# Kernel tuning notes

Measured on AMD Instinct MI355X. Metric: run time of the kernel, lower is better.

## Reference

```python
import jax, jax.numpy as jnp
import numpy as np

DELTA = 1e-3  # inverse-distance kernel smoothing from NEC paper
NUM_NEIGHBOURS = 50


def setup_inputs() -> dict:
    key = jax.random.key(0)
    k1, k2, k3 = jax.random.split(key, 3)
    B, C, D = 1024, 500000, 64
    return {
        "keys": jax.random.normal(k1, (B, D), dtype=jnp.float32),
        "table_keys": jax.random.normal(k2, (C, D), dtype=jnp.float32),
        "table_values": jax.random.normal(k3, (C,), dtype=jnp.float32),
    }


def reference(keys, table_keys, table_values):
    # Brute-force kNN search: squared L2 distances [B, C]
    d2 = (
        jnp.sum(keys * keys, axis=1, keepdims=True)
        - 2.0 * (keys @ table_keys.T)
        + jnp.sum(table_keys * table_keys, axis=1)[None, :]
    )
    _, idx = jax.lax.top_k(-d2, NUM_NEIGHBOURS)  # [B, K] smallest distances

    neighbours = table_keys[idx]  # [B, K, D] gather
    # recompute exact squared distances against gathered neighbours
    sq = jnp.sum((keys[:, None, :] - neighbours) ** 2, axis=2)  # [B, K]
    w = 1.0 / (sq + DELTA)
    w = w / jnp.sum(w, axis=1, keepdims=True)
    v = table_values[idx]  # [B, K]
    return jnp.sum(w * v, axis=1)  # [B]
```

## Files before the change

kernel.cpp:

```cpp
#include <hip/hip_runtime.h>
#include <math.h>


#define DELTA_SMOOTH 1e-3f
#define K_NEIGH 50
#define MAXCAP 8192
#define SAMPLE 2048
#define SAMPLE_TARGET 6
#define NBINS 256
#define MARGIN 0.75f
#define MARGIN_Q 26
#define RPB 1024
#define QTILE 512
#define SDEPTH 8
#define LW 768
#define NQ 1024

typedef __attribute__((ext_vector_type(8))) short short8;
typedef __attribute__((ext_vector_type(4))) float f32x4;

__device__ __forceinline__ unsigned f2bf(float f) {
  unsigned u = __float_as_uint(f);
  return ((u + 0x7fffu + ((u >> 16) & 1u)) >> 16) & 0xffffu;
}

__global__ __launch_bounds__(256) void qthresh_kernel(
    const float* __restrict__ keys, const float* __restrict__ tk,
    float* __restrict__ thr, float* __restrict__ qnorm, int C) {
  int q = blockIdx.x;
  __shared__ __align__(16) float kq[64];
  __shared__ unsigned hist[NBINS];
  __shared__ float qn_sh;
  __shared__ unsigned wsum[4];
  __shared__ int bstar_sh;
  int tid = threadIdx.x;
  int lane = tid & 63;
  int wid = tid >> 6;
  if (tid < 64) kq[tid] = keys[(size_t)q * 64 + tid];
  hist[tid] = 0u;
  if (tid == 0) bstar_sh = NBINS - 1;
  __syncthreads();
  if (tid < 64) {
    float v = kq[tid];
    float s = v * v;
    #pragma unroll
    for (int off = 32; off > 0; off >>= 1) s += __shfl_down(s, off);
    if (tid == 0) qn_sh = s;
  }
  __syncthreads();
  float qn = qn_sh;
  int kc = lane & 3;
  const float4* kq4 = (const float4*)kq;
  float4 kf[4];
  #pragma unroll
  for (int j = 0; j < 4; ++j) kf[j] = kq4[kc * 4 + j];
  int S = SAMPLE < C ? SAMPLE : C;
  for (int r = wid * (S >> 2) + (lane >> 2); r < (wid + 1) * (S >> 2); r += 16) {
    const float4* trow = (const float4*)(tk + (size_t)r * 64 + kc * 16);
    float a0 = 0.f, a1 = 0.f, sq = 0.f;
    #pragma unroll
    for (int j = 0; j < 4; ++j) {
      float4 tvv = trow[j];
      float4 kv = kf[j];
      a0 += kv.x * tvv.x + kv.y * tvv.y;
      a1 += kv.z * tvv.z + kv.w * tvv.w;
      sq += tvv.x * tvv.x + tvv.y * tvv.y + tvv.z * tvv.z + tvv.w * tvv.w;
    }
    float s = a0 + a1;
    s += __shfl_xor(s, 1); s += __shfl_xor(s, 2);
    sq += __shfl_xor(sq, 1); sq += __shfl_xor(sq, 2);
    if (kc == 0) {
      float d2 = qn + sq - 2.f * s;
      int b = (int)d2;
      b = b < 0 ? 0 : (b > NBINS - 1 ? NBINS - 1 : b);
      atomicAdd(&hist[b], 1u);
    }
  }
  __syncthreads();
  unsigned h = hist[tid];
  unsigned p = h;
  #pragma unroll
  for (int off = 1; off < 64; off <<= 1) {
    unsigned v = __shfl_up(p, off);
    if (lane >= off) p += v;
  }
  if (lane == 63) wsum[wid] = p;
  __syncthreads();
  unsigned add = 0;
  for (int w2 = 0; w2 < wid; ++w2) add += wsum[w2];
  p += add;
  if (p >= (unsigned)SAMPLE_TARGET && p - h < (unsigned)SAMPLE_TARGET) bstar_sh = tid;
  __syncthreads();
  if (tid == 0) {
    thr[q] = (float)(bstar_sh + 1) + MARGIN - qn;
    qnorm[q] = qn;
  }
}

__global__ __launch_bounds__(512, 4) void filter_mfma_kernel(
    const float* __restrict__ keys, const float* __restrict__ tk,
    const float* __restrict__ thr, const float* __restrict__ qnorm,
    int* __restrict__ cnt, unsigned* __restrict__ candi, int C, int cap) {
  __shared__ float tnstage[64];
  __shared__ float thr_lds[QTILE];
  __shared__ float qn_lds[QTILE];
  __shared__ unsigned scnt[QTILE];
  __shared__ unsigned sbuf[QTILE * SDEPTH];
  __shared__ __align__(16) unsigned char bstage[64 * 128];

  int tid = threadIdx.x;
  int qt = blockIdx.x & 1;
  int chunk = blockIdx.x >> 1;
  int qbase = qt * QTILE;
  int rstart = chunk * RPB;

  thr_lds[tid] = thr[qbase + tid];
  qn_lds[tid] = qnorm[qbase + tid];
  scnt[tid] = 0u;

  int lane = tid & 63;
  int wq = tid >> 6;
  int l15 = lane & 15;
  int quad = lane >> 4;

  short8 afrag[4][2];
  #pragma unroll
  for (int mt = 0; mt < 4; ++mt) {
    const float* kp = keys + (size_t)(qbase + wq * 64 + mt * 16 + l15) * 64 + quad * 8;
    #pragma unroll
    for (int s = 0; s < 2; ++s) {
      float4 x = *(const float4*)(kp + s * 32);
      float4 y = *(const float4*)(kp + s * 32 + 4);
      short8 a;
      a[0] = (short)f2bf(x.x); a[1] = (short)f2bf(x.y);
      a[2] = (short)f2bf(x.z); a[3] = (short)f2bf(x.w);
      a[4] = (short)f2bf(y.x); a[5] = (short)f2bf(y.y);
      a[6] = (short)f2bf(y.z); a[7] = (short)f2bf(y.w);
      afrag[mt][s] = a;
    }
  }
  __syncthreads();

  float hq[4];
  #pragma unroll
  for (int mt = 0; mt < 4; ++mt) {
    float h0 = thr_lds[wq * 64 + mt * 16 + quad * 4 + 0];
    float h1 = thr_lds[wq * 64 + mt * 16 + quad * 4 + 1];
    float h2 = thr_lds[wq * 64 + mt * 16 + quad * 4 + 2];
    float h3 = thr_lds[wq * 64 + mt * 16 + quad * 4 + 3];
    hq[mt] = fmaxf(fmaxf(h0, h1), fmaxf(h2, h3));
  }

  int srow = tid >> 3;
  int scol = tid & 7;
  unsigned sbyte = (unsigned)(srow * 128 + ((scol ^ (srow & 7)) << 4));

  const int ITERS = RPB / 64;
  int r0 = rstart + srow; if (r0 > C - 1) r0 = C - 1;
  float4 pa = *(const float4*)(tk + (size_t)r0 * 64 + scol * 8);
  float4 pb = *(const float4*)(tk + (size_t)r0 * 64 + scol * 8 + 4);

  f32x4 zero4 = {0.f, 0.f, 0.f, 0.f};

  for (int it = 0; it < ITERS; ++it) {
    float part = pa.x * pa.x + pa.y * pa.y + pa.z * pa.z + pa.w * pa.w
               + pb.x * pb.x + pb.y * pb.y + pb.z * pb.z + pb.w * pb.w;
    part += __shfl_xor(part, 1);
    part += __shfl_xor(part, 2);
    part += __shfl_xor(part, 4);
    if ((tid & 7) == 0) tnstage[srow] = part;
    uint4 u;
    u.x = f2bf(pa.x) | (f2bf(pa.y) << 16);
    u.y = f2bf(pa.z) | (f2bf(pa.w) << 16);
    u.z = f2bf(pb.x) | (f2bf(pb.y) << 16);
    u.w = f2bf(pb.z) | (f2bf(pb.w) << 16);
    *(uint4*)(bstage + sbyte) = u;
    __syncthreads();
    if (it + 1 < ITERS) {
      int rn = rstart + (it + 1) * 64 + srow; if (rn > C - 1) rn = C - 1;
      pa = *(const float4*)(tk + (size_t)rn * 64 + scol * 8);
      pb = *(const float4*)(tk + (size_t)rn * 64 + scol * 8 + 4);
    }
    #pragma unroll
    for (int half = 0; half < 2; ++half) {
      short8 b[2][2];
      #pragma unroll
      for (int tt = 0; tt < 2; ++tt) {
        int nloc = half * 32 + tt * 16 + l15;
        #pragma unroll
        for (int s = 0; s < 2; ++s) {
          int c = s * 4 + quad;
          unsigned addr = (unsigned)(nloc * 128 + ((c ^ (nloc & 7)) << 4));
          b[tt][s] = *(const short8*)(bstage + addr);
        }
      }
      f32x4 acc[4][2];
      #pragma unroll
      for (int mt = 0; mt < 4; ++mt) {
        #pragma unroll
        for (int tt = 0; tt < 2; ++tt) {
          f32x4 a0 = __builtin_amdgcn_mfma_f32_16x16x32_bf16(afrag[mt][0], b[tt][0], zero4, 0, 0, 0);
          acc[mt][tt] = __builtin_amdgcn_mfma_f32_16x16x32_bf16(afrag[mt][1], b[tt][1], a0, 0, 0, 0);
        }
      }
      #pragma unroll
      for (int tt = 0; tt < 2; ++tt) {
        float tn = tnstage[half * 32 + tt * 16 + l15];
        int n = rstart + it * 64 + half * 32 + tt * 16 + l15;
        #pragma unroll
        for (int mt = 0; mt < 4; ++mt) {
          float d0 = fmaf(-2.f, acc[mt][tt][0], tn);
          float d1 = fmaf(-2.f, acc[mt][tt][1], tn);
          float d2 = fmaf(-2.f, acc[mt][tt][2], tn);
          float d3 = fmaf(-2.f, acc[mt][tt][3], tn);
          float mn4 = fminf(fminf(d0, d1), fminf(d2, d3));
          if (mn4 < hq[mt]) {
            float dd[4] = {d0, d1, d2, d3};
            #pragma unroll
            for (int r = 0; r < 4; ++r) {
              int ql = wq * 64 + mt * 16 + quad * 4 + r;
              if (dd[r] < thr_lds[ql] && n < C) {
                float d2f = dd[r] + qn_lds[ql];
                int d2q = (int)(d2f * 16.f);
                d2q = d2q < 0 ? 0 : (d2q > 8191 ? 8191 : d2q);
                unsigned v = ((unsigned)d2q << 19) | (unsigned)n;
                unsigned p = atomicAdd(&scnt[ql], 1u);
                if (p < SDEPTH) {
                  sbuf[ql * SDEPTH + p] = v;
                } else {
                  int g = atomicAdd(&cnt[qbase + ql], 1);
                  if (g < cap) candi[(size_t)(qbase + ql) * cap + g] = v;
                }
              }
            }
          }
        }
      }
    }
    __syncthreads();
  }
  int m = (int)scnt[tid];
  if (m > SDEPTH) m = SDEPTH;
  if (m > 0) {
    int base = atomicAdd(&cnt[qbase + tid], m);
    for (int j = 0; j < m; ++j) {
      int g = base + j;
      if (g < cap) candi[(size_t)(qbase + tid) * cap + g] = sbuf[tid * SDEPTH + j];
    }
  }
}

__global__ __launch_bounds__(256) void select_kernel(
    const float* __restrict__ keys, const float* __restrict__ tk,
    const float* __restrict__ tv, const int* __restrict__ cnt,
    const unsigned* __restrict__ candi, float* __restrict__ out, int cap) {
  int q = blockIdx.x;
  __shared__ unsigned hist[NBINS];
  __shared__ unsigned wsum[4];
  __shared__ unsigned minq_sh;
  __shared__ int b50_sh;
  __shared__ int lidx[LW];
  __shared__ unsigned ed2[LW];
  __shared__ int m_sh;
  __shared__ float redw[4], redwv[4];
  int tid = threadIdx.x;
  int lane = tid & 63;
  int wid = tid >> 6;
  int n = cnt[q];
  if (n > cap) n = cap;
  hist[tid] = 0u;
  if (tid == 0) { minq_sh = 0xffffffffu; b50_sh = NBINS - 1; m_sh = 0; }
  __syncthreads();
  const unsigned* cv = candi + (size_t)q * cap;
  unsigned mn = 0xffffffffu;
  for (int i = tid; i < n; i += 256) { unsigned d = cv[i] >> 19; if (d < mn) mn = d; }
  #pragma unroll
  for (int off = 1; off < 64; off <<= 1) { unsigned o = __shfl_xor(mn, off); if (o < mn) mn = o; }
  if (lane == 0) atomicMin(&minq_sh, mn);
  __syncthreads();
  unsigned base = minq_sh;
  for (int i = tid; i < n; i += 256) {
    unsigned d = (cv[i] >> 19) - base;
    unsigned b = d >> 1; if (b > NBINS - 1) b = NBINS - 1;
    atomicAdd(&hist[b], 1u);
  }
  __syncthreads();
  unsigned h = hist[tid];
  unsigned p = h;
  #pragma unroll
  for (int off = 1; off < 64; off <<= 1) {
    unsigned v = __shfl_up(p, off);
    if (lane >= off) p += v;
  }
  if (lane == 63) wsum[wid] = p;
  __syncthreads();
  unsigned add = 0;
  for (int w2 = 0; w2 < wid; ++w2) add += wsum[w2];
  p += add;
  if (p >= (unsigned)K_NEIGH && p - h < (unsigned)K_NEIGH) b50_sh = tid;
  __syncthreads();
  unsigned Tq = base + (((unsigned)(b50_sh + 1)) << 1) + MARGIN_Q;
  for (int i = tid; i < n; i += 256) {
    unsigned v = cv[i];
    if ((v >> 19) <= Tq) {
      int p2 = atomicAdd(&m_sh, 1);
      if (p2 < LW) lidx[p2] = (int)(v & 0x7ffffu);
    }
  }
  __syncthreads();
  int m = m_sh; if (m > LW) m = LW;
  float kqv = keys[(size_t)q * 64 + lane];
  for (int i0 = wid * 4; i0 < m; i0 += 16) {
    int mm = m - i0; if (mm > 4) mm = 4;
    int idx[4]; float t[4];
    for (int u = 0; u < mm; ++u) idx[u] = lidx[i0 + u];
    for (int u = 0; u < mm; ++u) t[u] = tk[(size_t)idx[u] * 64 + lane];
    for (int u = 0; u < mm; ++u) {
      float d = t[u] - kqv;
      float s = d * d;
      #pragma unroll
      for (int off = 1; off < 64; off <<= 1) s += __shfl_xor(s, off);
      if (lane == 0) ed2[i0 + u] = __float_as_uint(s);
    }
  }
  __syncthreads();
  float accw = 0.f, accwv = 0.f;
  for (int i = tid; i < m; i += 256) {
    unsigned long long key = ((unsigned long long)ed2[i] << 19) | (unsigned)lidx[i];
    int rank = 0;
    for (int j = 0; j < m; ++j) {
      unsigned long long kj = ((unsigned long long)ed2[j] << 19) | (unsigned)lidx[j];
      rank += (kj < key) ? 1 : 0;
    }
    if (rank < K_NEIGH) {
      float d2 = __uint_as_float(ed2[i]);
      float w = 1.f / (d2 + DELTA_SMOOTH);
      accw += w;
      accwv += w * tv[lidx[i]];
    }
  }
  #pragma unroll
  for (int off = 1; off < 64; off <<= 1) {
    accw += __shfl_xor(accw, off);
    accwv += __shfl_xor(accwv, off);
  }
  if (lane == 0) { redw[wid] = accw; redwv[wid] = accwv; }
  __syncthreads();
  if (tid == 0) {
    float sw = redw[0] + redw[1] + redw[2] + redw[3];
    float swv = redwv[0] + redwv[1] + redwv[2] + redwv[3];
    out[q] = swv / sw;
  }
}

extern "C" void kernel_launch(void* const* d_in, const int* in_sizes, int n_in,
                              void* d_out, int out_size, void* d_ws, size_t ws_size,
                              hipStream_t stream) {
  const float* keys = (const float*)d_in[0];
  const float* tk   = (const float*)d_in[1];
  const float* tv   = (const float*)d_in[2];
  float* out = (float*)d_out;
  int B = in_sizes[0] / 64;
  int C = in_sizes[2];

  char* w = (char*)d_ws;
  float* thr = (float*)w;  w += (size_t)B * 4;
  float* qn  = (float*)w;  w += (size_t)B * 4;
  int*   cnt = (int*)w;    w += (size_t)B * 4;
  size_t used = (size_t)(w - (char*)d_ws);
  size_t avail = ws_size > used ? ws_size - used : 0;
  int cap = (int)(avail / (4ull * (size_t)B));
  if (cap > MAXCAP) cap = MAXCAP;
  if (cap < 1) cap = 1;
  unsigned* candi = (unsigned*)w;

  hipMemsetAsync(cnt, 0, (size_t)B * 4, stream);
  qthresh_kernel<<<B, 256, 0, stream>>>(keys, tk, thr, qn, C);
  int nchunks = (C + RPB - 1) / RPB;
  filter_mfma_kernel<<<nchunks * 2, 512, 0, stream>>>(keys, tk, thr, qn,
                                                      cnt, candi, C, cap);
  select_kernel<<<B, 256, 0, stream>>>(keys, tk, tv, cnt, candi, out, cap);
}
```

Before: 450.0 us.

## Pre-convert table to bf16 MFMA layout and stage candidates in LDS

Adds a conversion kernel that writes the table keys once as bf16 in an MFMA-fragment-friendly layout, along with precomputed half squared norms. A new filter kernel then loads B fragments straight from global memory, with no per-block fp32-to-bf16 conversion or LDS staging. The select kernel also caches up to 4096 candidates in LDS so its three passes do not reread global memory. The cost is an extra pass over the table and a larger workspace. If the workspace is too small, the code falls back to the old path.

```diff
diff --git a/kernel.cpp b/kernel.cpp
--- a/kernel.cpp
+++ b/kernel.cpp
@@ -14,7 +14,7 @@
 #define QTILE 512
 #define SDEPTH 8
 #define LW 768
-#define NQ 1024
+#define CVL 4096
 
 typedef __attribute__((ext_vector_type(8))) short short8;
 typedef __attribute__((ext_vector_type(4))) float f32x4;
@@ -22,6 +22,28 @@
 __device__ __forceinline__ unsigned f2bf(float f) {
   unsigned u = __float_as_uint(f);
   return ((u + 0x7fffu + ((u >> 16) & 1u)) >> 16) & 0xffffu;
+}
+
+__global__ __launch_bounds__(256) void convert_kernel(
+    const float* __restrict__ tk, uint4* __restrict__ tkbf,
+    float* __restrict__ tnh2, int C, int padded) {
+  int t = blockIdx.x * 256 + threadIdx.x;
+  int r = t >> 3;
+  if (r >= padded) return;
+  int c = t & 7;
+  int rs = r < C ? r : C - 1;
+  const float4* src = (const float4*)(tk + (size_t)rs * 64 + c * 8);
+  float4 a = src[0], b = src[1];
+  float sq = a.x * a.x + a.y * a.y + a.z * a.z + a.w * a.w
+           + b.x * b.x + b.y * b.y + b.z * b.z + b.w * b.w;
+  sq += __shfl_xor(sq, 1); sq += __shfl_xor(sq, 2); sq += __shfl_xor(sq, 4);
+  if (c == 0) tnh2[r] = sq * 0.5f;
+  uint4 u;
+  u.x = f2bf(a.x) | (f2bf(a.y) << 16);
+  u.y = f2bf(a.z) | (f2bf(a.w) << 16);
+  u.z = f2bf(b.x) | (f2bf(b.y) << 16);
+  u.w = f2bf(b.z) | (f2bf(b.w) << 16);
+  tkbf[t] = u;
 }
 
 __global__ __launch_bounds__(256) void qthresh_kernel(
@@ -94,6 +116,130 @@
   if (tid == 0) {
     thr[q] = (float)(bstar_sh + 1) + MARGIN - qn;
     qnorm[q] = qn;
+  }
+}
+
+__global__ __launch_bounds__(512, 4) void filter_mfma_fast(
+    const uint4* __restrict__ tkbf, const float* __restrict__ keys,
+    const float* __restrict__ tnh2, const float* __restrict__ thr,
+    const float* __restrict__ qnorm, int* __restrict__ cnt,
+    unsigned* __restrict__ candi, int C, int cap) {
+  __shared__ float tnh_lds[RPB];
+  __shared__ float thr_lds[QTILE];
+  __shared__ float qn_lds[QTILE];
+  __shared__ unsigned scnt[QTILE];
+  __shared__ unsigned sbuf[QTILE * SDEPTH];
+
+  int tid = threadIdx.x;
+  int qt = blockIdx.x & 1;
+  int chunk = blockIdx.x >> 1;
+  int qbase = qt * QTILE;
+  int rstart = chunk * RPB;
+
+  tnh_lds[tid] = tnh2[rstart + tid];
+  tnh_lds[tid + 512] = tnh2[rstart + tid + 512];
+  thr_lds[tid] = thr[qbase + tid];
+  qn_lds[tid] = qnorm[qbase + tid];
+  scnt[tid] = 0u;
+
+  int lane = tid & 63;
+  int wq = tid >> 6;
+  int l15 = lane & 15;
+  int quad = lane >> 4;
+
+  short8 afrag[4][2];
+  #pragma unroll
+  for (int mt = 0; mt < 4; ++mt) {
+    const float* kp = keys + (size_t)(qbase + wq * 64 + mt * 16 + l15) * 64 + quad * 8;
+    #pragma unroll
+    for (int s = 0; s < 2; ++s) {
+      float4 x = *(const float4*)(kp + s * 32);
+      float4 y = *(const float4*)(kp + s * 32 + 4);
+      short8 a;
+      a[0] = (short)f2bf(x.x); a[1] = (short)f2bf(x.y);
+      a[2] = (short)f2bf(x.z); a[3] = (short)f2bf(x.w);
+      a[4] = (short)f2bf(y.x); a[5] = (short)f2bf(y.y);
+      a[6] = (short)f2bf(y.z); a[7] = (short)f2bf(y.w);
+      afrag[mt][s] = a;
+    }
+  }
+  __syncthreads();
+
+  float htr[4][4], hmax[4];
+  #pragma unroll
+  for (int mt = 0; mt < 4; ++mt) {
+    #pragma unroll
+    for (int r = 0; r < 4; ++r)
+      htr[mt][r] = thr_lds[wq * 64 + mt * 16 + quad * 4 + r] * 0.5f;
+    hmax[mt] = fmaxf(fmaxf(htr[mt][0], htr[mt][1]), fmaxf(htr[mt][2], htr[mt][3]));
+  }
+
+  int lbase = l15 * 8 + quad;
+  const uint4* gt = tkbf + (size_t)(rstart >> 6) * 512 + lbase;
+
+  f32x4 zero4 = {0.f, 0.f, 0.f, 0.f};
+  const int ITERS = RPB / 64;
+
+  for (int it = 0; it < ITERS; ++it) {
+    const uint4* tp = gt + it * 512;
+    #pragma unroll
+    for (int half = 0; half < 2; ++half) {
+      short8 b[2][2];
+      #pragma unroll
+      for (int tt = 0; tt < 2; ++tt)
+        #pragma unroll
+        for (int s = 0; s < 2; ++s)
+          b[tt][s] = *(const short8*)(tp + half * 256 + tt * 128 + s * 4);
+      f32x4 acc[4][2];
+      #pragma unroll
+      for (int mt = 0; mt < 4; ++mt) {
+        #pragma unroll
+        for (int tt = 0; tt < 2; ++tt) {
+          f32x4 a0 = __builtin_amdgcn_mfma_f32_16x16x32_bf16(afrag[mt][0], b[tt][0], zero4, 0, 0, 0);
+          acc[mt][tt] = __builtin_amdgcn_mfma_f32_16x16x32_bf16(afrag[mt][1], b[tt][1], a0, 0, 0, 0);
+        }
+      }
+      #pragma unroll
+      for (int tt = 0; tt < 2; ++tt) {
+        int rloc = it * 64 + half * 32 + tt * 16 + l15;
+        float tnh = tnh_lds[rloc];
+        int n = rstart + rloc;
+        #pragma unroll
+        for (int mt = 0; mt < 4; ++mt) {
+          float mx4 = fmaxf(fmaxf(acc[mt][tt][0], acc[mt][tt][1]),
+                            fmaxf(acc[mt][tt][2], acc[mt][tt][3]));
+          if (mx4 + hmax[mt] > tnh) {
+            #pragma unroll
+            for (int r = 0; r < 4; ++r) {
+              if (acc[mt][tt][r] + htr[mt][r] > tnh && n < C) {
+                int ql = wq * 64 + mt * 16 + quad * 4 + r;
+                float d2f = 2.f * (tnh - acc[mt][tt][r]) + qn_lds[ql];
+                int d2q = (int)(d2f * 16.f);
+                d2q = d2q < 0 ? 0 : (d2q > 8191 ? 8191 : d2q);
+                unsigned v = ((unsigned)d2q << 19) | (unsigned)n;
+                unsigned p = atomicAdd(&scnt[ql], 1u);
+                if (p < SDEPTH) {
+                  sbuf[ql * SDEPTH + p] = v;
+                } else {
+                  int g = atomicAdd(&cnt[qbase + ql], 1);
+                  if (g < cap) candi[(size_t)(qbase + ql) * cap + g] = v;
+                }
+              }
+            }
+          }
+        }
+      }
+    }
+  }
+  __syncthreads();
+  int m = (int)scnt[tid];
+  if (m > SDEPTH) m = SDEPTH;
+  if (m > 0) {
+    int base = atomicAdd(&cnt[qbase + tid], m);
+    for (int j = 0; j < m; ++j) {
+      int g = base + j;
+      if (g < cap) candi[(size_t)(qbase + tid) * cap + g] = sbuf[tid * SDEPTH + j];
+    }
   }
 }
 
@@ -255,6 +401,7 @@
     const float* __restrict__ tv, const int* __restrict__ cnt,
     const unsigned* __restrict__ candi, float* __restrict__ out, int cap) {
   int q = blockIdx.x;
+  __shared__ unsigned cvl[CVL];
   __shared__ unsigned hist[NBINS];
   __shared__ unsigned wsum[4];
   __shared__ unsigned minq_sh;
@@ -273,14 +420,19 @@
   __syncthreads();
   const unsigned* cv = candi + (size_t)q * cap;
   unsigned mn = 0xffffffffu;
-  for (int i = tid; i < n; i += 256) { unsigned d = cv[i] >> 19; if (d < mn) mn = d; }
+  for (int i = tid; i < n; i += 256) {
+    unsigned v = cv[i];
+    if (i < CVL) cvl[i] = v;
+    unsigned d = v >> 19; if (d < mn) mn = d;
+  }
   #pragma unroll
   for (int off = 1; off < 64; off <<= 1) { unsigned o = __shfl_xor(mn, off); if (o < mn) mn = o; }
   if (lane == 0) atomicMin(&minq_sh, mn);
   __syncthreads();
   unsigned base = minq_sh;
   for (int i = tid; i < n; i += 256) {
-    unsigned d = (cv[i] >> 19) - base;
+    unsigned v = (i < CVL) ? cvl[i] : cv[i];
+    unsigned d = (v >> 19) - base;
     unsigned b = d >> 1; if (b > NBINS - 1) b = NBINS - 1;
     atomicAdd(&hist[b], 1u);
   }
@@ -301,7 +453,7 @@
   __syncthreads();
   unsigned Tq = base + (((unsigned)(b50_sh + 1)) << 1) + MARGIN_Q;
   for (int i = tid; i < n; i += 256) {
-    unsigned v = cv[i];
+    unsigned v = (i < CVL) ? cvl[i] : cv[i];
     if ((v >> 19) <= Tq) {
       int p2 = atomicAdd(&m_sh, 1);
       if (p2 < LW) lidx[p2] = (int)(v & 0x7ffffu);
@@ -363,21 +515,40 @@
   int B = in_sizes[0] / 64;
   int C = in_sizes[2];
 
+  int nchunks = (C + RPB - 1) / RPB;
+  int padded = nchunks * RPB;
+
   char* w = (char*)d_ws;
   float* thr = (float*)w;  w += (size_t)B * 4;
   float* qn  = (float*)w;  w += (size_t)B * 4;
   int*   cnt = (int*)w;    w += (size_t)B * 4;
-  size_t used = (size_t)(w - (char*)d_ws);
-  size_t avail = ws_size > used ? ws_size - used : 0;
-  int cap = (int)(avail / (4ull * (size_t)B));
-  if (cap > MAXCAP) cap = MAXCAP;
-  if (cap < 1) cap = 1;
-  unsigned* candi = (unsigned*)w;
+
+  size_t fixed = (size_t)(w - (char*)d_ws);
+  size_t fast_need = fixed + (size_t)padded * 128 + (size_t)padded * 4
+                   + 2048ull * (size_t)B * 4;
+  bool fast = ws_size >= fast_need;
 
   hipMemsetAsync(cnt, 0, (size_t)B * 4, stream);
   qthresh_kernel<<<B, 256, 0, stream>>>(keys, tk, thr, qn, C);
-  int nchunks = (C + RPB - 1) / RPB;
-  filter_mfma_kernel<<<nchunks * 2, 512, 0, stream>>>(keys, tk, thr, qn,
+
+  if (fast) {
+    uint4* tkbf  = (uint4*)w;             w += (size_t)padded * 128;
+    float* tnh2  = (float*)w;             w += (size_t)padded * 4;
+    size_t used = (size_t)(w - (char*)d_ws);
+    int cap = (int)((ws_size - used) / (4ull * (size_t)B));
+    if (cap > MAXCAP) cap = MAXCAP;
+    unsigned* candi = (unsigned*)w;
+    convert_kernel<<<padded / 32, 256, 0, stream>>>(tk, tkbf, tnh2, C, padded);
+    filter_mfma_fast<<<nchunks * 2, 512, 0, stream>>>(tkbf, keys, tnh2, thr, qn,
                                                       cnt, candi, C, cap);
-  select_kernel<<<B, 256, 0, stream>>>(keys, tk, tv, cnt, candi, out, cap);
-}
+    select_kernel<<<B, 256, 0, stream>>>(keys, tk, tv, cnt, candi, out, cap);
+  } else {
+    int cap = (int)((ws_size - fixed) / (4ull * (size_t)B));
+    if (cap > MAXCAP) cap = MAXCAP;
+    if (cap < 1) cap = 1;
+    unsigned* candi = (unsigned*)w;
+    filter_mfma_kernel<<<nchunks * 2, 512, 0, stream>>>(keys, tk, thr, qn,
+                                                        cnt, candi, C, cap);
+    select_kernel<<<B, 256, 0, stream>>>(keys, tk, tv, cnt, candi, out, cap);
+  }
+}
```

New measurement: 492.7 us. +9.5%, slower.
